# Kernel tuning notes

Hardware: AMD Instinct MI355X
Metric: run time of the kernel (lower is better)

Reference implementation:

```python
import jax, jax.numpy as jnp
import numpy as np

N = 100000   # nodes
E = 1600000  # edges (avg degree 16)
F_IN, H1, H2, H3, C = 500, 200, 100, 40, 3


def setup_inputs() -> dict:
    key = jax.random.key(0)
    ks = jax.random.split(key, 10)
    def w(k, shape, fan_in):
        return jax.random.normal(k, shape, dtype=jnp.float32) / np.sqrt(fan_in)
    return {
        "x": jax.random.normal(ks[0], (N, F_IN), dtype=jnp.float32),
        "edge_index": jax.random.randint(ks[1], (2, E), 0, N, dtype=jnp.int32),
        "W1": w(ks[2], (H1, F_IN), F_IN), "b1": jnp.zeros((H1,), jnp.float32),
        "W1b": w(ks[3], (H2, H1), H1),  "b1b": jnp.zeros((H2,), jnp.float32),
        "W2b": w(ks[4], (H3, H2), H2),  "b2b": jnp.zeros((H3,), jnp.float32),
        "W2": w(ks[5], (C, H3), H3),    "b2": jnp.zeros((C,), jnp.float32),
    }


def _gcn_conv(x, W, b, src, dst, norm_e, n):
    # GCNConv: linear transform, then normalized scatter-add aggregation, then bias
    h = x @ W.T                                   # [N, out]
    msgs = h[src] * norm_e[:, None]               # [E+N, out] gathered, normalized
    out = jax.ops.segment_sum(msgs, dst, num_segments=n)
    return out + b


def reference(x, edge_index, W1, b1, W1b, b1b, W2b, b2b, W2, b2):
    n = x.shape[0]
    loop = jnp.arange(n, dtype=edge_index.dtype)
    src = jnp.concatenate([edge_index[0], loop])  # add self-loops (GCNConv default)
    dst = jnp.concatenate([edge_index[1], loop])
    # symmetric normalization: deg computed on target nodes, norm = d^-1/2[src]*d^-1/2[dst]
    deg = jax.ops.segment_sum(jnp.ones_like(dst, dtype=x.dtype), dst, num_segments=n)
    dinv = jnp.where(deg > 0, jax.lax.rsqrt(deg), 0.0)
    norm_e = dinv[src] * dinv[dst]

    # dropout(p=0.5, training=self.training) is identity at inference
    h = jax.nn.relu(_gcn_conv(x, W1, b1, src, dst, norm_e, n))
    h = jax.nn.relu(_gcn_conv(h, W1b, b1b, src, dst, norm_e, n))
    h = jax.nn.relu(_gcn_conv(h, W2b, b2b, src, dst, norm_e, n))
    return _gcn_conv(h, W2, b2, src, dst, norm_e, n)
```

## Files before the change

kernel.cpp:

```cpp
#include <hip/hip_runtime.h>


#define DEV __device__ __forceinline__

typedef __attribute__((ext_vector_type(8))) short short8;
typedef __attribute__((ext_vector_type(8))) _Float16 f16x8;
typedef __attribute__((ext_vector_type(4))) float f32x4;
typedef __attribute__((ext_vector_type(4))) _Float16 f16x4;

DEV void gload_lds16(const void* g, void* l) {
    __builtin_amdgcn_global_load_lds(
        (const __attribute__((address_space(1))) unsigned int*)g,
        (__attribute__((address_space(3))) unsigned int*)l, 16, 0, 0);
}


__global__ void k_init(int* __restrict__ cnt, int n) {
    int i = blockIdx.x * 256 + threadIdx.x;
    if (i < n) cnt[i] = 0;
}

__global__ void k_count(const int* __restrict__ dst, int* __restrict__ cnt,
                        int* __restrict__ rank, int E) {
    int e = blockIdx.x * 256 + threadIdx.x;
    if (e < E) rank[e] = atomicAdd(&cnt[dst[e]], 1);
}

__global__ void k_scan1(const int* __restrict__ cnt, int* __restrict__ row_start,
                        int* __restrict__ partial, float* __restrict__ dinv, int n) {
    __shared__ int sdata[256];
    int base = blockIdx.x * 1024;
    int t = threadIdx.x;
    int v[4]; int sum = 0;
#pragma unroll
    for (int j = 0; j < 4; ++j) {
        int idx = base + t * 4 + j;
        v[j] = (idx < n) ? (cnt[idx] + 1) : 0;
        if (idx < n) dinv[idx] = rsqrtf((float)v[j]);
        sum += v[j];
    }
    sdata[t] = sum;
    __syncthreads();
    for (int off = 1; off < 256; off <<= 1) {
        int x = (t >= off) ? sdata[t - off] : 0;
        __syncthreads();
        sdata[t] += x;
        __syncthreads();
    }
    int excl = sdata[t] - sum;
#pragma unroll
    for (int j = 0; j < 4; ++j) {
        int idx = base + t * 4 + j;
        if (idx < n) row_start[idx] = excl;
        excl += v[j];
    }
    if (t == 255) partial[blockIdx.x] = sdata[255];
}

__global__ void k_scan2(int* __restrict__ partial, int nb) {
    __shared__ int s[128];
    int t = threadIdx.x;
    int v = (t < nb) ? partial[t] : 0;
    s[t] = v;
    __syncthreads();
    for (int off = 1; off < 128; off <<= 1) {
        int x = (t >= off) ? s[t - off] : 0;
        __syncthreads();
        s[t] += x;
        __syncthreads();
    }
    if (t < nb) partial[t] = s[t] - v;
}

__global__ void k_scan3(int* __restrict__ row_start, const int* __restrict__ partial,
                        int n, int total) {
    int i = blockIdx.x * 256 + threadIdx.x;
    if (i < n) row_start[i] += partial[i >> 10];
    if (i == 0) row_start[n] = total;
}

__global__ void k_fill(const int* __restrict__ src, const int* __restrict__ dst,
                       const int* __restrict__ row_start, const int* __restrict__ cnt,
                       const int* __restrict__ rank, int* __restrict__ csr_src,
                       int E, int n) {
    int i = blockIdx.x * 256 + threadIdx.x;
    int total = E + n;
    if (i >= total) return;
    int s, pos;
    if (i < E) {
        s = src[i];
        int d = dst[i];
        pos = row_start[d] + rank[i];
    } else {
        s = i - E;
        pos = row_start[s] + cnt[s];
    }
    csr_src[pos] = s;
}


__global__ void k_wcvt16(const float* __restrict__ W, int N, int K,
                         unsigned short* __restrict__ Wh, int NPAD, int KPAD) {
    int i = blockIdx.x * 256 + threadIdx.x;
    if (i >= NPAD * KPAD) return;
    int r = i / KPAD, k = i - r * KPAD;
    float x = (r < N && k < K) ? W[r * K + k] : 0.f;
    Wh[i] = __builtin_bit_cast(unsigned short, (_Float16)x);
}

__global__ void k_wdec16(const float* __restrict__ W, int N, int K,
                         unsigned short* __restrict__ Wh, unsigned short* __restrict__ Wl,
                         int NPAD, int KPAD) {
    int i = blockIdx.x * 256 + threadIdx.x;
    if (i >= NPAD * KPAD) return;
    int r = i / KPAD, k = i - r * KPAD;
    float x = (r < N && k < K) ? W[r * K + k] : 0.f;
    _Float16 h = (_Float16)x;
    _Float16 l = (_Float16)((x - (float)h) * 2048.0f);
    Wh[i] = __builtin_bit_cast(unsigned short, h);
    Wl[i] = __builtin_bit_cast(unsigned short, l);
}


struct A8 { f32x4 lo, hi; };

template <int NFC, int KPH, int NPH, int HILO, int MODE, typename AT>
__global__ __launch_bounds__(512, 4)
void gemm_res(const AT* __restrict__ A, int lda, int M, int K,
              const unsigned short* __restrict__ Wh,
              const unsigned short* __restrict__ Wl,
              const float* __restrict__ dinv,
              _Float16* __restrict__ H16, int ldh, int Nout) {
    constexpr int NPAD = NFC * 16;
    constexpr int KP   = KPH * NPH;
    constexpr int CHH  = NPAD * KPH / 8;
    constexpr int CHT  = CHH * (1 + HILO);
    constexpr int NIT  = (CHT + 511) / 512;
    constexpr int SB   = NPAD * 64;
    constexpr int HB   = CHH * 16;
    constexpr int SPP  = KPH / 32;
    constexpr int NS   = SPP * NPH;
    constexpr int D    = 3;
    __shared__ char lds[CHT * 16];

    const int tid  = threadIdx.x;
    const int wv   = tid >> 6;
    const int lane = tid & 63;
    const int lr   = lane & 15;
    const int kq   = lane >> 4;
    const int m0   = blockIdx.y * 128;
    const int col0 = blockIdx.x * NPAD;

    const unsigned short* WhB = Wh + (size_t)col0 * KP;
    const unsigned short* WlB = Wl + (size_t)col0 * KP;

    auto stageW = [&](int p) {
#pragma unroll
        for (int i = 0; i < NIT; ++i) {
            int c = tid + i * 512;
            if ((CHT % 512 == 0) || (c < CHT)) {
                int h  = (HILO && c >= CHH) ? 1 : 0;
                int cc = c - h * CHH;
                int st = cc / (NPAD * 4);
                int rm = cc - st * (NPAD * 4);
                int r  = rm >> 2;
                int sl = rm & 3;
                int gs = sl ^ (r & 3);
                const unsigned short* gp = (h ? WlB : WhB)
                    + (size_t)r * KP + p * KPH + st * 32 + gs * 8;
                gload_lds16(gp, lds + (size_t)c * 16);
            }
        }
    };

    int arow = m0 + wv * 16 + lr;
    if (arow >= M) arow = M - 1;
    const AT* Arow = A + (size_t)arow * lda;

    auto loadA32 = [&](int s) -> A8 {
        A8 o;
        int kb = s * 32 + kq * 8;
        if (kb + 8 <= K) {
            const float* ap = (const float*)Arow + kb;
            o.lo = *(const f32x4*)ap;
            o.hi = *(const f32x4*)(ap + 4);
        } else {
#pragma unroll
            for (int i = 0; i < 4; ++i) {
                int k0 = kb + i, k1 = kb + 4 + i;
                o.lo[i] = (k0 < K) ? (float)Arow[k0] : 0.f;
                o.hi[i] = (k1 < K) ? (float)Arow[k1] : 0.f;
            }
        }
        return o;
    };
    auto loadA16 = [&](int s) -> short8 {
        int kb = s * 32 + kq * 8;
        if (kb + 8 <= K) return *(const short8*)((const unsigned short*)Arow + kb);
        short8 o;
        const unsigned short* ap = (const unsigned short*)Arow;
#pragma unroll
        for (int i = 0; i < 8; ++i) o[i] = (kb + i < K) ? (short)ap[kb + i] : (short)0;
        return o;
    };
    auto cvtA = [&](const A8& a) -> f16x8 {
        f16x8 o;
#pragma unroll
        for (int i = 0; i < 4; ++i) {
            o[i]     = (_Float16)a.lo[i];
            o[4 + i] = (_Float16)a.hi[i];
        }
        return o;
    };

    stageW(0);
    A8 ab[D]; short8 hb[D];
#pragma unroll
    for (int p = 0; p < D; ++p) {
        if (p < NS) {
            if constexpr (MODE == 0) ab[p] = loadA32(p);
            else                     hb[p] = loadA16(p);
        }
    }

    f32x4 ac[NFC], al[NFC];
#pragma unroll
    for (int f = 0; f < NFC; ++f) {
        ac[f] = (f32x4){0.f, 0.f, 0.f, 0.f};
        al[f] = (f32x4){0.f, 0.f, 0.f, 0.f};
    }

    __syncthreads();

    const int ro = lr * 64 + ((kq ^ (lr & 3)) << 4);

#pragma unroll
    for (int p = 0; p < NPH; ++p) {
#pragma unroll
        for (int sl = 0; sl < SPP; ++sl) {
            const int s = p * SPP + sl;
            f16x8 a0;
            if constexpr (MODE == 0) a0 = cvtA(ab[s % D]);
            else                     a0 = __builtin_bit_cast(f16x8, hb[s % D]);

            if (s + D < NS) {
                if constexpr (MODE == 0) ab[s % D] = loadA32(s + D);
                else                     hb[s % D] = loadA16(s + D);
            }

            const char* bb = lds + sl * SB;
#pragma unroll
            for (int f = 0; f < NFC; ++f) {
                f16x8 bh = __builtin_bit_cast(f16x8, *(const short8*)(bb + f * 1024 + ro));
                ac[f] = __builtin_amdgcn_mfma_f32_16x16x32_f16(a0, bh, ac[f], 0, 0, 0);
                if constexpr (HILO) {
                    f16x8 bl = __builtin_bit_cast(f16x8, *(const short8*)(bb + HB + f * 1024 + ro));
                    al[f] = __builtin_amdgcn_mfma_f32_16x16x32_f16(a0, bl, al[f], 0, 0, 0);
                }
            }
        }
        if (p + 1 < NPH) {
            __syncthreads();
            stageW(p + 1);
            __syncthreads();
        }
    }

    const int rbase = m0 + wv * 16 + kq * 4;
    float dv[4];
#pragma unroll
    for (int j = 0; j < 4; ++j) {
        int row = rbase + j;
        dv[j] = (row < M) ? dinv[row] : 0.f;
    }
#pragma unroll
    for (int f = 0; f < NFC; ++f) {
        int col = col0 + f * 16 + lr;
        if (col >= Nout) continue;
#pragma unroll
        for (int j = 0; j < 4; ++j) {
            int row = rbase + j;
            if (row >= M) continue;
            float v = ac[f][j];
            if constexpr (HILO) v += al[f][j] * (1.0f / 2048.0f);
            H16[(size_t)row * ldh + col] = (_Float16)(v * dv[j]);
        }
    }
}


template <int F, int VEC, bool RELU>
__global__ __launch_bounds__(256)
void agg_f16(const _Float16* __restrict__ h, const int* __restrict__ row_start,
             const int* __restrict__ csr_src, const float* __restrict__ dinv,
             const float* __restrict__ bias, _Float16* __restrict__ out, int n,
             int ldo) {
    constexpr int LPN = F / VEC;
    constexpr int NPW = 64 / LPN;
    int wave = blockIdx.x * 4 + (threadIdx.x >> 6);
    int lane = threadIdx.x & 63;
    int sub  = lane / LPN;
    int fi   = lane - sub * LPN;
    int node = wave * NPW + sub;
    if (sub >= NPW || node >= n) return;
    int f = fi * VEC;
    const _Float16* hf = h + f;

    f32x4 acc0 = {0.f, 0.f, 0.f, 0.f};
    f32x4 acc1 = {0.f, 0.f, 0.f, 0.f};

    auto addv = [&](const _Float16* p) {
        if constexpr (VEC == 8) {
            f16x8 v = *(const f16x8*)p;
            f16x4 vl, vh;
#pragma unroll
            for (int j = 0; j < 4; ++j) { vl[j] = v[j]; vh[j] = v[4 + j]; }
            acc0 += __builtin_convertvector(vl, f32x4);
            acc1 += __builtin_convertvector(vh, f32x4);
        } else {
            f16x4 v = *(const f16x4*)p;
            acc0 += __builtin_convertvector(v, f32x4);
        }
    };

    int e0 = row_start[node], e1 = row_start[node + 1];
    int e = e0;
    for (; e + 4 <= e1; e += 4) {
        int s0 = csr_src[e + 0];
        int s1 = csr_src[e + 1];
        int s2 = csr_src[e + 2];
        int s3 = csr_src[e + 3];
        const _Float16* p0 = &hf[(size_t)s0 * F];
        const _Float16* p1 = &hf[(size_t)s1 * F];
        const _Float16* p2 = &hf[(size_t)s2 * F];
        const _Float16* p3 = &hf[(size_t)s3 * F];
        addv(p0); addv(p1); addv(p2); addv(p3);
    }
    for (; e < e1; ++e) addv(&hf[(size_t)csr_src[e] * F]);

    float dn = dinv[node];
    if constexpr (VEC == 8) {
        f32x4 b0 = *(const f32x4*)&bias[f];
        f32x4 b1 = *(const f32x4*)&bias[f + 4];
        acc0 = acc0 * dn + b0;
        acc1 = acc1 * dn + b1;
        if (RELU) {
#pragma unroll
            for (int j = 0; j < 4; ++j) { acc0[j] = fmaxf(acc0[j], 0.f); acc1[j] = fmaxf(acc1[j], 0.f); }
        }
        f16x8 o;
#pragma unroll
        for (int j = 0; j < 4; ++j) { o[j] = (_Float16)acc0[j]; o[4 + j] = (_Float16)acc1[j]; }
        *(f16x8*)&out[(size_t)node * ldo + f] = o;
    } else {
        f32x4 b4 = *(const f32x4*)&bias[f];
        acc0 = acc0 * dn + b4;
        if (RELU) {
#pragma unroll
            for (int j = 0; j < 4; ++j) acc0[j] = fmaxf(acc0[j], 0.f);
        }
        f16x4 o;
#pragma unroll
        for (int j = 0; j < 4; ++j) o[j] = (_Float16)acc0[j];
        *(f16x4*)&out[(size_t)node * ldo + f] = o;
    }
}


__global__ void gemm_small(const _Float16* __restrict__ A, const float* __restrict__ B,
                           const float* __restrict__ dinv, float* __restrict__ C,
                           int M, int K) {
    int m = blockIdx.x * 256 + threadIdx.x;
    if (m >= M) return;
    float a0 = 0.f, a1 = 0.f, a2 = 0.f;
    for (int k = 0; k < K; ++k) {
        float a = (float)A[(size_t)m * K + k];
        a0 += a * B[0 * K + k];
        a1 += a * B[1 * K + k];
        a2 += a * B[2 * K + k];
    }
    float dv = dinv[m];
    C[(size_t)m * 3 + 0] = a0 * dv;
    C[(size_t)m * 3 + 1] = a1 * dv;
    C[(size_t)m * 3 + 2] = a2 * dv;
}

__global__ void agg_f3(const float* __restrict__ h, const int* __restrict__ row_start,
                       const int* __restrict__ csr_src, const float* __restrict__ dinv,
                       const float* __restrict__ bias, float* __restrict__ out, int n) {
    int i = blockIdx.x * 256 + threadIdx.x;
    if (i >= n * 3) return;
    int node = i / 3;
    int f = i - node * 3;
    float acc = 0.f;
    int e1 = row_start[node + 1];
    for (int e = row_start[node]; e < e1; ++e) {
        int s = csr_src[e];
        acc += h[(size_t)s * 3 + f];
    }
    out[i] = acc * dinv[node] + bias[f];
}


extern "C" void kernel_launch(void* const* d_in, const int* in_sizes, int n_in,
                              void* d_out, int out_size, void* d_ws, size_t ws_size,
                              hipStream_t stream) {
    const float* x   = (const float*)d_in[0];
    const int*   ei  = (const int*)d_in[1];
    const float* W1  = (const float*)d_in[2];
    const float* b1  = (const float*)d_in[3];
    const float* W1b = (const float*)d_in[4];
    const float* b1b = (const float*)d_in[5];
    const float* W2b = (const float*)d_in[6];
    const float* b2b = (const float*)d_in[7];
    const float* W2  = (const float*)d_in[8];
    const float* b2  = (const float*)d_in[9];
    float* out = (float*)d_out;

    const int F_IN = 500, H1 = 200, H2 = 100, H3 = 40;
    const int N = in_sizes[0] / F_IN;
    const int E = in_sizes[1] / 2;
    const int* src = ei;
    const int* dst = ei + E;

    size_t off = 0;
    auto alloc = [&](size_t bytes) -> void* {
        void* p = (char*)d_ws + off;
        off += (bytes + 255) & ~(size_t)255;
        return p;
    };
    int*   cnt       = (int*)  alloc((size_t)N * 4);
    int*   row_start = (int*)  alloc((size_t)(N + 1) * 4);
    int*   rank      = (int*)  alloc((size_t)E * 4);
    int*   partial   = (int*)  alloc(128 * 4);
    float* dinv      = (float*)alloc((size_t)N * 4);
    int*   csr_src   = (int*)  alloc((size_t)(E + N) * 4);
    unsigned short* wh1 = (unsigned short*)alloc(224 * 512 * 2);
    unsigned short* wh2 = (unsigned short*)alloc(128 * 256 * 2);
    unsigned short* wl2 = (unsigned short*)alloc(128 * 256 * 2);
    unsigned short* wh3 = (unsigned short*)alloc( 64 * 128 * 2);
    unsigned short* wl3 = (unsigned short*)alloc( 64 * 128 * 2);
    _Float16* h16   = (_Float16*)alloc((size_t)N * H1 * 2);
    _Float16* act16 = (_Float16*)alloc((size_t)N * H1 * 2);
    float*    bufC  = (float*)   alloc((size_t)N * 3 * 4);

    int gN  = (N + 255) / 256;
    int gE  = (E + 255) / 256;
    int gEN = (E + N + 255) / 256;
    int nb  = (N + 1023) / 1024;

    k_init <<<gN, 256, 0, stream>>>(cnt, N);
    k_count<<<gE, 256, 0, stream>>>(dst, cnt, rank, E);
    k_scan1<<<nb, 256, 0, stream>>>(cnt, row_start, partial, dinv, N);
    k_scan2<<<1, 128, 0, stream>>>(partial, nb);
    k_scan3<<<gN, 256, 0, stream>>>(row_start, partial, N, E + N);
    k_fill <<<gEN, 256, 0, stream>>>(src, dst, row_start, cnt, rank, csr_src, E, N);

    k_wcvt16<<<(224 * 512 + 255) / 256, 256, 0, stream>>>(W1,  H1, F_IN, wh1, 224, 512);
    k_wdec16<<<(128 * 256 + 255) / 256, 256, 0, stream>>>(W1b, H2, H1, wh2, wl2, 128, 256);
    k_wdec16<<<( 64 * 128 + 255) / 256, 256, 0, stream>>>(W2b, H3, H2, wh3, wl3,  64, 128);

    const int gR = (N + 127) / 128;

    gemm_res<14, 128, 4, 0, 0, float><<<dim3(1, gR), 512, 0, stream>>>(
        x, F_IN, N, F_IN, wh1, wh1, dinv, h16, H1, H1);
    {
        int waves = (N + 1) / 2, blocks = (waves + 3) / 4;
        agg_f16<200, 8, true><<<blocks, 256, 0, stream>>>(h16, row_start, csr_src, dinv,
                                                          b1, act16, N, 200);
    }
    gemm_res<4, 128, 2, 1, 1, _Float16><<<dim3(2, gR), 512, 0, stream>>>(
        act16, 200, N, H1, wh2, wl2, dinv, h16, H2, H2);
    agg_f16<100, 4, true><<<(N / 2 + 3) / 4, 256, 0, stream>>>(h16, row_start, csr_src, dinv,
                                                               b1b, act16, N, 112);
    gemm_res<4, 128, 1, 1, 1, _Float16><<<dim3(1, gR), 512, 0, stream>>>(
        act16, 112, N, H2, wh3, wl3, dinv, h16, H3, H3);
    {
        int waves = (N + 11) / 12, blocks = (waves + 3) / 4;
        agg_f16<40, 8, true><<<blocks, 256, 0, stream>>>(h16, row_start, csr_src, dinv,
                                                         b2b, act16, N, 40);
    }
    gemm_small<<<(N + 255) / 256, 256, 0, stream>>>(act16, W2, dinv, bufC, N, H3);
    agg_f3<<<(N * 3 + 255) / 256, 256, 0, stream>>>(bufC, row_start, csr_src, dinv,
                                                    b2, out, N);
}
```

Before: 507.0 us.

## Fuse preprocessing kernels and fold CSR fill into first GEMM

Merges edge counting and the three weight conversions into one prep kernel, replaces the init kernel with a memset, and moves the CSR fill scatter into the start of the first GEMM so it overlaps with the GEMM blocks. This cuts the number of kernel launches and the serial tail of small kernels. It also lowers the GEMM pipeline depth constant D from 3 to 2. The risks are that the scattered fill work adds latency at the front of each GEMM block, and that the smaller pipeline depth may hide memory latency less well.

```diff
diff --git a/kernel.cpp b/kernel.cpp
--- a/kernel.cpp
+++ b/kernel.cpp
@@ -15,16 +15,47 @@
 }
 
 
-__global__ void k_init(int* __restrict__ cnt, int n) {
+__global__ void k_prep(const int* __restrict__ dst, int* __restrict__ cnt,
+                       int* __restrict__ rank, int E,
+                       const float* __restrict__ W1, unsigned short* __restrict__ wh1,
+                       const float* __restrict__ W1b, unsigned short* __restrict__ wh2,
+                       unsigned short* __restrict__ wl2,
+                       const float* __restrict__ W2b, unsigned short* __restrict__ wh3,
+                       unsigned short* __restrict__ wl3) {
+    const int SZ1 = 224 * 512, SZ2 = 128 * 256, SZ3 = 64 * 128;
     int i = blockIdx.x * 256 + threadIdx.x;
-    if (i < n) cnt[i] = 0;
-}
-
-__global__ void k_count(const int* __restrict__ dst, int* __restrict__ cnt,
-                        int* __restrict__ rank, int E) {
-    int e = blockIdx.x * 256 + threadIdx.x;
-    if (e < E) rank[e] = atomicAdd(&cnt[dst[e]], 1);
-}
+    if (i < E) {
+        rank[i] = atomicAdd(&cnt[dst[i]], 1);
+        return;
+    }
+    i -= E;
+    if (i < SZ1) {
+        int r = i >> 9, k = i & 511;
+        float x = (r < 200 && k < 500) ? W1[r * 500 + k] : 0.f;
+        wh1[i] = __builtin_bit_cast(unsigned short, (_Float16)x);
+        return;
+    }
+    i -= SZ1;
+    if (i < SZ2) {
+        int r = i >> 8, k = i & 255;
+        float x = (r < 100 && k < 200) ? W1b[r * 200 + k] : 0.f;
+        _Float16 h = (_Float16)x;
+        _Float16 l = (_Float16)((x - (float)h) * 2048.0f);
+        wh2[i] = __builtin_bit_cast(unsigned short, h);
+        wl2[i] = __builtin_bit_cast(unsigned short, l);
+        return;
+    }
+    i -= SZ2;
+    if (i < SZ3) {
+        int r = i >> 7, k = i & 127;
+        float x = (r < 40 && k < 100) ? W2b[r * 100 + k] : 0.f;
+        _Float16 h = (_Float16)x;
+        _Float16 l = (_Float16)((x - (float)h) * 2048.0f);
+        wh3[i] = __builtin_bit_cast(unsigned short, h);
+        wl3[i] = __builtin_bit_cast(unsigned short, l);
+    }
+}
+
 
 __global__ void k_scan1(const int* __restrict__ cnt, int* __restrict__ row_start,
                         int* __restrict__ partial, float* __restrict__ dinv, int n) {
@@ -79,58 +110,19 @@
     if (i == 0) row_start[n] = total;
 }
 
-__global__ void k_fill(const int* __restrict__ src, const int* __restrict__ dst,
-                       const int* __restrict__ row_start, const int* __restrict__ cnt,
-                       const int* __restrict__ rank, int* __restrict__ csr_src,
-                       int E, int n) {
-    int i = blockIdx.x * 256 + threadIdx.x;
-    int total = E + n;
-    if (i >= total) return;
-    int s, pos;
-    if (i < E) {
-        s = src[i];
-        int d = dst[i];
-        pos = row_start[d] + rank[i];
-    } else {
-        s = i - E;
-        pos = row_start[s] + cnt[s];
-    }
-    csr_src[pos] = s;
-}
-
-
-__global__ void k_wcvt16(const float* __restrict__ W, int N, int K,
-                         unsigned short* __restrict__ Wh, int NPAD, int KPAD) {
-    int i = blockIdx.x * 256 + threadIdx.x;
-    if (i >= NPAD * KPAD) return;
-    int r = i / KPAD, k = i - r * KPAD;
-    float x = (r < N && k < K) ? W[r * K + k] : 0.f;
-    Wh[i] = __builtin_bit_cast(unsigned short, (_Float16)x);
-}
-
-__global__ void k_wdec16(const float* __restrict__ W, int N, int K,
-                         unsigned short* __restrict__ Wh, unsigned short* __restrict__ Wl,
-                         int NPAD, int KPAD) {
-    int i = blockIdx.x * 256 + threadIdx.x;
-    if (i >= NPAD * KPAD) return;
-    int r = i / KPAD, k = i - r * KPAD;
-    float x = (r < N && k < K) ? W[r * K + k] : 0.f;
-    _Float16 h = (_Float16)x;
-    _Float16 l = (_Float16)((x - (float)h) * 2048.0f);
-    Wh[i] = __builtin_bit_cast(unsigned short, h);
-    Wl[i] = __builtin_bit_cast(unsigned short, l);
-}
-
 
 struct A8 { f32x4 lo, hi; };
 
-template <int NFC, int KPH, int NPH, int HILO, int MODE, typename AT>
+template <int NFC, int KPH, int NPH, int HILO, int MODE, int DOFILL, typename AT>
 __global__ __launch_bounds__(512, 4)
 void gemm_res(const AT* __restrict__ A, int lda, int M, int K,
               const unsigned short* __restrict__ Wh,
               const unsigned short* __restrict__ Wl,
               const float* __restrict__ dinv,
-              _Float16* __restrict__ H16, int ldh, int Nout) {
+              _Float16* __restrict__ H16, int ldh, int Nout,
+              const int* __restrict__ fsrc, const int* __restrict__ fdst,
+              const int* __restrict__ frows, const int* __restrict__ fcnt,
+              const int* __restrict__ frank, int* __restrict__ fcsr, int fE, int fN) {
     constexpr int NPAD = NFC * 16;
     constexpr int KP   = KPH * NPH;
     constexpr int CHH  = NPAD * KPH / 8;
@@ -140,7 +132,7 @@
     constexpr int HB   = CHH * 16;
     constexpr int SPP  = KPH / 32;
     constexpr int NS   = SPP * NPH;
-    constexpr int D    = 3;
+    constexpr int D    = 2;
     __shared__ char lds[CHT * 16];
 
     const int tid  = threadIdx.x;
@@ -150,6 +142,25 @@
     const int kq   = lane >> 4;
     const int m0   = blockIdx.y * 128;
     const int col0 = blockIdx.x * NPAD;
+
+    if constexpr (DOFILL) {
+        int total = fE + fN;
+        int nb    = gridDim.y;
+        int per   = (total + nb - 1) / nb;
+        int base  = blockIdx.y * per;
+        int end   = base + per; if (end > total) end = total;
+        for (int i = base + tid; i < end; i += 512) {
+            int s, pos;
+            if (i < fE) {
+                s = fsrc[i];
+                pos = frows[fdst[i]] + frank[i];
+            } else {
+                s = i - fE;
+                pos = frows[s] + fcnt[s];
+            }
+            fcsr[pos] = s;
+        }
+    }
 
     const unsigned short* WhB = Wh + (size_t)col0 * KP;
     const unsigned short* WlB = Wl + (size_t)col0 * KP;
@@ -444,37 +455,38 @@
     _Float16* act16 = (_Float16*)alloc((size_t)N * H1 * 2);
     float*    bufC  = (float*)   alloc((size_t)N * 3 * 4);
 
-    int gN  = (N + 255) / 256;
-    int gE  = (E + 255) / 256;
-    int gEN = (E + N + 255) / 256;
-    int nb  = (N + 1023) / 1024;
-
-    k_init <<<gN, 256, 0, stream>>>(cnt, N);
-    k_count<<<gE, 256, 0, stream>>>(dst, cnt, rank, E);
+    int gN = (N + 255) / 256;
+    int nb = (N + 1023) / 1024;
+
+    hipMemsetAsync(cnt, 0, (size_t)N * 4, stream);
+    {
+        int total = E + 224 * 512 + 128 * 256 + 64 * 128;
+        k_prep<<<(total + 255) / 256, 256, 0, stream>>>(dst, cnt, rank, E,
+                                                        W1, wh1, W1b, wh2, wl2,
+                                                        W2b, wh3, wl3);
+    }
     k_scan1<<<nb, 256, 0, stream>>>(cnt, row_start, partial, dinv, N);
     k_scan2<<<1, 128, 0, stream>>>(partial, nb);
     k_scan3<<<gN, 256, 0, stream>>>(row_start, partial, N, E + N);
-    k_fill <<<gEN, 256, 0, stream>>>(src, dst, row_start, cnt, rank, csr_src, E, N);
-
-    k_wcvt16<<<(224 * 512 + 255) / 256, 256, 0, stream>>>(W1,  H1, F_IN, wh1, 224, 512);
-    k_wdec16<<<(128 * 256 + 255) / 256, 256, 0, stream>>>(W1b, H2, H1, wh2, wl2, 128, 256);
-    k_wdec16<<<( 64 * 128 + 255) / 256, 256, 0, stream>>>(W2b, H3, H2, wh3, wl3,  64, 128);
 
     const int gR = (N + 127) / 128;
 
-    gemm_res<14, 128, 4, 0, 0, float><<<dim3(1, gR), 512, 0, stream>>>(
-        x, F_IN, N, F_IN, wh1, wh1, dinv, h16, H1, H1);
+    gemm_res<14, 128, 4, 0, 0, 1, float><<<dim3(1, gR), 512, 0, stream>>>(
+        x, F_IN, N, F_IN, wh1, wh1, dinv, h16, H1, H1,
+        src, dst, row_start, cnt, rank, csr_src, E, N);
     {
         int waves = (N + 1) / 2, blocks = (waves + 3) / 4;
         agg_f16<200, 8, true><<<blocks, 256, 0, stream>>>(h16, row_start, csr_src, dinv,
                                                           b1, act16, N, 200);
     }
-    gemm_res<4, 128, 2, 1, 1, _Float16><<<dim3(2, gR), 512, 0, stream>>>(
-        act16, 200, N, H1, wh2, wl2, dinv, h16, H2, H2);
+    gemm_res<4, 128, 2, 1, 1, 0, _Float16><<<dim3(2, gR), 512, 0, stream>>>(
+        act16, 200, N, H1, wh2, wl2, dinv, h16, H2, H2,
+        nullptr, nullptr, nullptr, nullptr, nullptr, nullptr, 0, 0);
     agg_f16<100, 4, true><<<(N / 2 + 3) / 4, 256, 0, stream>>>(h16, row_start, csr_src, dinv,
                                                                b1b, act16, N, 112);
-    gemm_res<4, 128, 1, 1, 1, _Float16><<<dim3(1, gR), 512, 0, stream>>>(
-        act16, 112, N, H2, wh3, wl3, dinv, h16, H3, H3);
+    gemm_res<4, 128, 1, 1, 1, 0, _Float16><<<dim3(1, gR), 512, 0, stream>>>(
+        act16, 112, N, H2, wh3, wl3, dinv, h16, H3, H3,
+        nullptr, nullptr, nullptr, nullptr, nullptr, nullptr, 0, 0);
     {
         int waves = (N + 11) / 12, blocks = (waves + 3) / 4;
         agg_f16<40, 8, true><<<blocks, 256, 0, stream>>>(h16, row_start, csr_src, dinv,
```

Result: faster. 494.0 us (-2.6%).
